# Kernel optimization log

Measured on AMD Instinct MI355X. Metric: run time of the kernel, lower is better.

Reference implementation:

```python
import jax, jax.numpy as jnp
import numpy as np

VOCAB = 200000
D = 128
B, P, R = 256, 64, 32
EPS = 1e-8


def _cos(a, b):
    # torch CosineSimilarity(dim=-1, eps=1e-8): clamp norms
    na = jnp.maximum(jnp.linalg.norm(a, axis=-1), EPS)
    nb = jnp.maximum(jnp.linalg.norm(b, axis=-1), EPS)
    return jnp.sum(a * b, axis=-1) / (na * nb)


def setup_inputs() -> dict:
    key = jax.random.key(0)
    ks = jax.random.split(key, 16)
    s = 1.0 / np.sqrt(D)
    inp = {
        "support_path": jax.random.randint(ks[0], (B, P, 3), 0, VOCAB - 1),
        "support_pair": jax.random.randint(ks[1], (B, 2), 0, VOCAB - 1),
        "support_relation_set": jax.random.randint(ks[2], (B, R), 0, VOCAB - 1),
        "emb": jax.random.normal(ks[3], (VOCAB, D), jnp.float32),
        "w_d_w": jax.random.uniform(ks[4], (D, D), jnp.float32, -s, s),
        "w_d_b": jax.random.uniform(ks[5], (D,), jnp.float32, -s, s),
        "w_e_w": jax.random.uniform(ks[6], (D, D), jnp.float32, -s, s),
        "w_e_b": jax.random.uniform(ks[7], (D,), jnp.float32, -s, s),
        "w_p_w": jax.random.uniform(ks[8], (D, D), jnp.float32, -s, s),
        "w_p_b": jax.random.uniform(ks[9], (D,), jnp.float32, -s, s),
        "e_u_w": jax.random.uniform(ks[10], (1, D), jnp.float32, -s, s),
        "e_u_b": jax.random.uniform(ks[11], (1,), jnp.float32, -s, s),
        "gru_w_ih": jax.random.uniform(ks[12], (3 * D, D), jnp.float32, -s, s),
        "gru_w_hh": jax.random.uniform(ks[13], (3 * D, D), jnp.float32, -s, s),
        "gru_b_ih": jax.random.uniform(ks[14], (3 * D,), jnp.float32, -s, s),
        "gru_b_hh": jax.random.uniform(ks[15], (3 * D,), jnp.float32, -s, s),
    }
    return inp


def _gru_cell(x, h, w_ih, w_hh, b_ih, b_hh):
    gi = x @ w_ih.T + b_ih
    gh = h @ w_hh.T + b_hh
    i_r, i_z, i_n = jnp.split(gi, 3, axis=-1)
    h_r, h_z, h_n = jnp.split(gh, 3, axis=-1)
    r = jax.nn.sigmoid(i_r + h_r)
    z = jax.nn.sigmoid(i_z + h_z)
    n = jnp.tanh(i_n + r * h_n)
    return (1.0 - z) * n + z * h


def reference(support_path, support_pair, support_relation_set, emb,
              w_d_w, w_d_b, w_e_w, w_e_b, w_p_w, w_p_b,
              e_u_w, e_u_b, gru_w_ih, gru_w_hh, gru_b_ih, gru_b_hh):
    head_emb = emb[support_pair[:, 0]]          # [B, D]
    tail_emb = emb[support_pair[:, 1]]          # [B, D]
    hts = _cos(head_emb, tail_emb)              # [B], head-tail sim per group

    rel_emb = emb[support_path]                 # [B, P, 3, D] per-step relation embeddings
    relset_emb = emb[support_relation_set]      # [B, R, D]

    # attention denominator over the group's relation set
    exp_set = jnp.exp(relset_emb @ e_u_w.T + e_u_b)        # [B, R, 1]
    sum_exp = jnp.sum(exp_set, axis=1, keepdims=True)      # [B, 1, 1]

    # entity_1/entity_2 are read from the path tensor in the original code
    e1 = rel_emb[:, :, 0, :]                                # [B, P, D]
    e2 = rel_emb[:, :, 1, :]
    h_b = head_emb[:, None, :]                              # [B, 1, D]
    t_b = tail_emb[:, None, :]
    sim_e1 = 0.5 * (_cos(h_b, e1) + _cos(t_b, e1))          # [B, P]
    sim_e2 = 0.5 * (_cos(h_b, e2) + _cos(t_b, e2))
    hts_b = hts[:, None]
    sim_rel = jnp.stack([
        0.5 * (hts_b + sim_e1),
        0.5 * (sim_e1 + sim_e2),
        0.5 * (hts_b + sim_e2),
    ], axis=-1)                                             # [B, P, 3]
    sim_dist = (1.0 - sim_rel) / 2.0                        # [B, P, 3]

    # attention score per path step
    e_score = jnp.exp(rel_emb @ e_u_w.T + e_u_b) / sum_exp[:, :, None, :]  # [B, P, 3, 1]

    d_in = rel_emb * sim_dist[..., None]
    e_in = rel_emb * e_score
    d_out = d_in @ w_d_w.T + w_d_b
    e_out = e_in @ w_e_w.T + w_e_b
    cost = 0.001 * jax.nn.relu(d_out + e_out)               # [B, P, 3, D]

    # GRU over 3 path steps, zero initial hidden
    rel_in = (rel_emb - cost) @ w_p_w.T + w_p_b             # [B, P, 3, D]
    x_steps = jnp.moveaxis(rel_in.reshape(B * P, 3, D), 1, 0)  # [3, B*P, D]

    def step(h, x):
        h2 = _gru_cell(x, h, gru_w_ih, gru_w_hh, gru_b_ih, gru_b_hh)
        return h2, None

    h0 = jnp.zeros((B * P, D), rel_in.dtype)
    h_final, _ = jax.lax.scan(step, h0, x_steps)
    return h_final.reshape(B, P, D)
```

## Files before the change

### kernel.cpp

```cpp
#include <hip/hip_runtime.h>
#include <cmath>

#define D_ 128
#define B_ 256
#define P_ 64
#define R_ 32
#define GROWS 192
#define EPS_ 1e-8f

typedef unsigned short u16;
typedef unsigned int   u32;
using bf16x8 = __attribute__((ext_vector_type(8))) __bf16;
using f32x4  = __attribute__((ext_vector_type(4))) float;

__device__ __forceinline__ float sigm_f(float x){ return 1.0f/(1.0f + __expf(-x)); }
__device__ __forceinline__ float tanh_f(float x){
    float e = __expf(2.0f*x);
    return 1.0f - 2.0f/(e + 1.0f);
}

__device__ __forceinline__ u16 f2b(float f){
    u32 u = __builtin_bit_cast(u32, f);
    u += 0x7fffu + ((u >> 16) & 1u);
    return (u16)(u >> 16);
}
__device__ __forceinline__ float b2f(u16 s){
    return __builtin_bit_cast(float, ((u32)s) << 16);
}
__device__ __forceinline__ bf16x8 pack8(float a0,float a1,float a2,float a3,
                                        float a4,float a5,float a6,float a7){
    uint4 r;
    r.x = (u32)f2b(a0) | ((u32)f2b(a1) << 16);
    r.y = (u32)f2b(a2) | ((u32)f2b(a3) << 16);
    r.z = (u32)f2b(a4) | ((u32)f2b(a5) << 16);
    r.w = (u32)f2b(a6) | ((u32)f2b(a7) << 16);
    return __builtin_bit_cast(bf16x8, r);
}
__device__ __forceinline__ bf16x8 ldg8(const u16* p){
    return __builtin_bit_cast(bf16x8, *(const uint4*)p);
}
__device__ __forceinline__ bf16x8 ldA(const u16* Xs, int row, int gk){
    return __builtin_bit_cast(bf16x8,
        *(const uint4*)(&Xs[row*128 + ((gk ^ (row & 7)) << 3)]));
}
__device__ __forceinline__ int swz_slot(int row, int col){
    return row*128 + (((col >> 3) ^ (row & 7)) << 3) + (col & 7);
}

__global__ __launch_bounds__(1024) void k_wcvt(
    const float* __restrict__ wd, const float* __restrict__ we,
    const float* __restrict__ wp, const float* __restrict__ wih,
    const float* __restrict__ whh,
    u16* __restrict__ wdb, u16* __restrict__ web, u16* __restrict__ wpb,
    u16* __restrict__ wib, u16* __restrict__ whb)
{
    int i = blockIdx.x*1024 + threadIdx.x;
    int e = i*8;
    const float* src; u16* dst; int off;
    if      (e < 16384) { src = wd;  dst = wdb; off = e; }
    else if (e < 32768) { src = we;  dst = web; off = e - 16384; }
    else if (e < 49152) { src = wp;  dst = wpb; off = e - 32768; }
    else if (e < 98304) { src = wih; dst = wib; off = e - 49152; }
    else                { src = whh; dst = whb; off = e - 98304; }
    float4 a = *(const float4*)(src + off);
    float4 b = *(const float4*)(src + off + 4);
    uint4 r;
    r.x = (u32)f2b(a.x) | ((u32)f2b(a.y) << 16);
    r.y = (u32)f2b(a.z) | ((u32)f2b(a.w) << 16);
    r.z = (u32)f2b(b.x) | ((u32)f2b(b.y) << 16);
    r.w = (u32)f2b(b.z) | ((u32)f2b(b.w) << 16);
    *(uint4*)(dst + off) = r;
}

__global__ __launch_bounds__(512,2) void k_mega(
    const int* __restrict__ pair, const int* __restrict__ relset,
    const int* __restrict__ path,
    const float* __restrict__ emb, const float* __restrict__ eu,
    const float* __restrict__ eub,
    const u16* __restrict__ wdb, const float* __restrict__ bd,
    const u16* __restrict__ web, const float* __restrict__ be,
    const u16* __restrict__ wpb, const float* __restrict__ bpv_,
    const u16* __restrict__ wib, const u16* __restrict__ whb,
    const float* __restrict__ bih, const float* __restrict__ bhh,
    float* __restrict__ out)
{
    __shared__ u16   Xs[GROWS*128];
    __shared__ u16   X2[GROWS*128];
    __shared__ u16   Hs[64*128];
    __shared__ int   pS[GROWS];
    __shared__ float pdh[GROWS], pdt[GROWS], pdu[GROWS], pnn[GROWS];
    __shared__ float sdS[GROWS], seS[GROWS];
    __shared__ float s_hts, s_hi, s_ti;
    __shared__ float s_part[8];

    const int b    = blockIdx.x;
    const int tid  = threadIdx.x;
    const int wave = tid >> 6, lane = tid & 63;
    const int lrow = lane & 15, lk8 = lane >> 4;
    const int col  = wave*16 + lrow;
    const float eb = eub[0];

    if (tid < GROWS) pS[tid] = path[b*GROWS + tid];
    bf16x8 fD[4], fE[4];
    #pragma unroll
    for (int ks = 0; ks < 4; ++ks) {
        const int gk = ks*4 + lk8;
        fD[ks] = ldg8(wdb + col*128 + gk*8);
        fE[ks] = ldg8(web + col*128 + gk*8);
    }
    const int ph = pair[2*b], ptl = pair[2*b+1];
    __syncthreads();

    {
        #pragma unroll
        for (int i = 0; i < 6; ++i) {
            int gid = i*512 + tid;
            int r = gid >> 4, g = gid & 15;
            const float* sp = emb + (size_t)pS[r]*128 + g*8;
            float4 f0 = *(const float4*)sp;
            float4 f1 = *(const float4*)(sp + 4);
            bf16x8 v = pack8(f0.x,f0.y,f0.z,f0.w, f1.x,f1.y,f1.z,f1.w);
            *(uint4*)(&Xs[r*128 + ((g ^ (r & 7)) << 3)]) = __builtin_bit_cast(uint4, v);
        }
        if (wave == 0) {
            float2 hv2 = *(const float2*)(emb + (size_t)ph*128 + 2*lane);
            float2 tv2 = *(const float2*)(emb + (size_t)ptl*128 + 2*lane);
            float dht = hv2.x*tv2.x + hv2.y*tv2.y;
            float dhh = hv2.x*hv2.x + hv2.y*hv2.y;
            float dtt = tv2.x*tv2.x + tv2.y*tv2.y;
            #pragma unroll
            for (int o = 32; o > 0; o >>= 1) {
                dht += __shfl_xor(dht, o);
                dhh += __shfl_xor(dhh, o);
                dtt += __shfl_xor(dtt, o);
            }
            if (lane == 0) {
                float hn = 1.f / fmaxf(sqrtf(dhh), EPS_);
                float tn = 1.f / fmaxf(sqrtf(dtt), EPS_);
                s_hts = dht*hn*tn;
                s_hi  = hn;
                s_ti  = tn;
            }
        }
        float2 uv2 = *(const float2*)(eu + 2*lane);
        float accs = 0.f;
        #pragma unroll
        for (int k = 0; k < 4; ++k) {
            const int ri = relset[b*R_ + wave*4 + k];
            float2 ev = *(const float2*)(emb + (size_t)ri*128 + 2*lane);
            float du = ev.x*uv2.x + ev.y*uv2.y;
            #pragma unroll
            for (int o = 32; o > 0; o >>= 1) du += __shfl_xor(du, o);
            accs += __expf(du + eb);
        }
        if (lane == 0) s_part[wave] = accs;
    }
    __syncthreads();

    {
        const int sub = lane >> 4, l16 = lane & 15;
        const float* hpq = emb + (size_t)ph*128  + l16*8;
        const float* tpq = emb + (size_t)ptl*128 + l16*8;
        const float* upq = eu + l16*8;
        float hq[8], tq[8], uq[8];
        {
            float4 a0 = *(const float4*)hpq, a1 = *(const float4*)(hpq+4);
            float4 b0 = *(const float4*)tpq, b1 = *(const float4*)(tpq+4);
            float4 c0 = *(const float4*)upq, c1 = *(const float4*)(upq+4);
            hq[0]=a0.x;hq[1]=a0.y;hq[2]=a0.z;hq[3]=a0.w;hq[4]=a1.x;hq[5]=a1.y;hq[6]=a1.z;hq[7]=a1.w;
            tq[0]=b0.x;tq[1]=b0.y;tq[2]=b0.z;tq[3]=b0.w;tq[4]=b1.x;tq[5]=b1.y;tq[6]=b1.z;tq[7]=b1.w;
            uq[0]=c0.x;uq[1]=c0.y;uq[2]=c0.z;uq[3]=c0.w;uq[4]=c1.x;uq[5]=c1.y;uq[6]=c1.z;uq[7]=c1.w;
        }
        #pragma unroll
        for (int i = 0; i < 6; ++i) {
            const int r = wave*24 + i*4 + sub;
            uint4 gv = *(const uint4*)(&Xs[r*128 + ((l16 ^ (r & 7)) << 3)]);
            float v[8];
            v[0]=b2f((u16)(gv.x&0xffff)); v[1]=b2f((u16)(gv.x>>16));
            v[2]=b2f((u16)(gv.y&0xffff)); v[3]=b2f((u16)(gv.y>>16));
            v[4]=b2f((u16)(gv.z&0xffff)); v[5]=b2f((u16)(gv.z>>16));
            v[6]=b2f((u16)(gv.w&0xffff)); v[7]=b2f((u16)(gv.w>>16));
            float dh=0.f, dt=0.f, du=0.f, nn=0.f;
            #pragma unroll
            for (int j = 0; j < 8; ++j) {
                dh = fmaf(v[j], hq[j], dh);
                dt = fmaf(v[j], tq[j], dt);
                du = fmaf(v[j], uq[j], du);
                nn = fmaf(v[j], v[j], nn);
            }
            #pragma unroll
            for (int o = 8; o > 0; o >>= 1) {
                dh += __shfl_xor(dh, o);
                dt += __shfl_xor(dt, o);
                du += __shfl_xor(du, o);
                nn += __shfl_xor(nn, o);
            }
            if (l16 == 0) { pdh[r]=dh; pdt[r]=dt; pdu[r]=du; pnn[r]=nn; }
        }
    }
    __syncthreads();

    if (tid < 64) {
        float is = 0.f;
        #pragma unroll
        for (int w = 0; w < 8; ++w) is += s_part[w];
        is = 1.f/is;
        const float hi = s_hi, ti = s_ti, ht = s_hts;
        const int r1 = 3*tid, r2 = r1+1, r3 = r1+2;
        float n1i = 1.f / fmaxf(sqrtf(pnn[r1]), EPS_);
        float n2i = 1.f / fmaxf(sqrtf(pnn[r2]), EPS_);
        float se1 = 0.5f*(pdh[r1]*hi + pdt[r1]*ti)*n1i;
        float se2 = 0.5f*(pdh[r2]*hi + pdt[r2]*ti)*n2i;
        sdS[r1] = (1.f - 0.5f*(ht  + se1))*0.5f;
        sdS[r2] = (1.f - 0.5f*(se1 + se2))*0.5f;
        sdS[r3] = (1.f - 0.5f*(ht  + se2))*0.5f;
        seS[r1] = expf(pdu[r1] + eb)*is;
        seS[r2] = expf(pdu[r2] + eb)*is;
        seS[r3] = expf(pdu[r3] + eb)*is;
    }
    __syncthreads();

    {
        const float bde = bd[col] + be[col];
        #pragma unroll 2
        for (int mt = 0; mt < 12; ++mt) {
            f32x4 aD = (f32x4){0,0,0,0}, aE = (f32x4){0,0,0,0};
            #pragma unroll
            for (int ks = 0; ks < 4; ++ks) {
                const int gk = ks*4 + lk8;
                bf16x8 a = ldA(Xs, mt*16 + lrow, gk);
                aD = __builtin_amdgcn_mfma_f32_16x16x32_bf16(a, fD[ks], aD, 0,0,0);
                aE = __builtin_amdgcn_mfma_f32_16x16x32_bf16(a, fE[ks], aE, 0,0,0);
            }
            #pragma unroll
            for (int rr = 0; rr < 4; ++rr) {
                const int row = mt*16 + lk8*4 + rr;
                const int sl  = swz_slot(row, col);
                float relv = b2f(Xs[sl]);
                float c = sdS[row]*aD[rr] + seS[row]*aE[rr] + bde;
                X2[sl] = f2b(relv - 1e-3f*fmaxf(c, 0.f));
            }
        }
    }
    __syncthreads();

    {
        bf16x8 fP[4];
        #pragma unroll
        for (int ks = 0; ks < 4; ++ks)
            fP[ks] = ldg8(wpb + col*128 + (ks*4 + lk8)*8);
        const float bpv = bpv_[col];
        #pragma unroll 2
        for (int mt = 0; mt < 12; ++mt) {
            f32x4 aP = (f32x4){0,0,0,0};
            #pragma unroll
            for (int ks = 0; ks < 4; ++ks) {
                const int gk = ks*4 + lk8;
                bf16x8 a = ldA(X2, mt*16 + lrow, gk);
                aP = __builtin_amdgcn_mfma_f32_16x16x32_bf16(a, fP[ks], aP, 0,0,0);
            }
            #pragma unroll
            for (int rr = 0; rr < 4; ++rr) {
                const int row = mt*16 + lk8*4 + rr;
                Xs[swz_slot(row, col)] = f2b(aP[rr] + bpv);
            }
        }
    }

    bf16x8 wR[4], wZ[4], wI[4];
    #pragma unroll
    for (int ks = 0; ks < 4; ++ks) {
        const int gk = ks*4 + lk8;
        wR[ks] = ldg8(wib +           col*128 + gk*8);
        wZ[ks] = ldg8(wib + 16384   + col*128 + gk*8);
        wI[ks] = ldg8(wib + 2*16384 + col*128 + gk*8);
    }
    const float brv = bih[col]       + bhh[col];
    const float bzv = bih[128 + col] + bhh[128 + col];
    const float biN = bih[256 + col];
    const float bhN = bhh[256 + col];
    __syncthreads();

    float hreg[4][4];
    f32x4 aR[4], aZ[4], aI[4], aH[4];

    #pragma unroll
    for (int m = 0; m < 4; ++m) { aR[m]=(f32x4){0,0,0,0}; aZ[m]=(f32x4){0,0,0,0}; aI[m]=(f32x4){0,0,0,0}; }
    #pragma unroll
    for (int ks = 0; ks < 4; ++ks) {
        const int gk = ks*4 + lk8;
        #pragma unroll
        for (int mt = 0; mt < 4; ++mt) {
            bf16x8 ax = ldA(Xs, 3*(mt*16 + lrow) + 0, gk);
            aR[mt] = __builtin_amdgcn_mfma_f32_16x16x32_bf16(ax, wR[ks], aR[mt], 0,0,0);
            aZ[mt] = __builtin_amdgcn_mfma_f32_16x16x32_bf16(ax, wZ[ks], aZ[mt], 0,0,0);
            aI[mt] = __builtin_amdgcn_mfma_f32_16x16x32_bf16(ax, wI[ks], aI[mt], 0,0,0);
        }
    }
    #pragma unroll
    for (int mt = 0; mt < 4; ++mt)
        #pragma unroll
        for (int rr = 0; rr < 4; ++rr) {
            const int row = mt*16 + lk8*4 + rr;
            float rv = sigm_f(aR[mt][rr] + brv);
            float zv = sigm_f(aZ[mt][rr] + bzv);
            float nn = tanh_f(aI[mt][rr] + biN + rv*bhN);
            float h2 = (1.f - zv)*nn;
            hreg[mt][rr] = h2;
            Hs[swz_slot(row, col)] = f2b(h2);
        }
    __syncthreads();

    #pragma unroll
    for (int t = 1; t < 3; ++t) {
        #pragma unroll
        for (int m = 0; m < 4; ++m) { aR[m]=(f32x4){0,0,0,0}; aZ[m]=(f32x4){0,0,0,0}; aI[m]=(f32x4){0,0,0,0}; aH[m]=(f32x4){0,0,0,0}; }
        #pragma unroll
        for (int ks = 0; ks < 4; ++ks) {
            const int gk = ks*4 + lk8;
            bf16x8 vRk = ldg8(whb +           col*128 + gk*8);
            bf16x8 vZk = ldg8(whb + 16384   + col*128 + gk*8);
            bf16x8 vHk = ldg8(whb + 2*16384 + col*128 + gk*8);
            #pragma unroll
            for (int mt = 0; mt < 4; ++mt) {
                bf16x8 ax = ldA(Xs, 3*(mt*16 + lrow) + t, gk);
                bf16x8 ah = ldA(Hs, mt*16 + lrow, gk);
                aR[mt] = __builtin_amdgcn_mfma_f32_16x16x32_bf16(ax, wR[ks], aR[mt], 0,0,0);
                aZ[mt] = __builtin_amdgcn_mfma_f32_16x16x32_bf16(ax, wZ[ks], aZ[mt], 0,0,0);
                aI[mt] = __builtin_amdgcn_mfma_f32_16x16x32_bf16(ax, wI[ks], aI[mt], 0,0,0);
                aR[mt] = __builtin_amdgcn_mfma_f32_16x16x32_bf16(ah, vRk, aR[mt], 0,0,0);
                aZ[mt] = __builtin_amdgcn_mfma_f32_16x16x32_bf16(ah, vZk, aZ[mt], 0,0,0);
                aH[mt] = __builtin_amdgcn_mfma_f32_16x16x32_bf16(ah, vHk, aH[mt], 0,0,0);
            }
        }
        __syncthreads();
        if (t < 2) {
            #pragma unroll
            for (int mt = 0; mt < 4; ++mt)
                #pragma unroll
                for (int rr = 0; rr < 4; ++rr) {
                    const int row = mt*16 + lk8*4 + rr;
                    float rv = sigm_f(aR[mt][rr] + brv);
                    float zv = sigm_f(aZ[mt][rr] + bzv);
                    float hn = aH[mt][rr] + bhN;
                    float nn = tanh_f(aI[mt][rr] + biN + rv*hn);
                    float h2 = (1.f - zv)*nn + zv*hreg[mt][rr];
                    hreg[mt][rr] = h2;
                    Hs[swz_slot(row, col)] = f2b(h2);
                }
            __syncthreads();
        } else {
            const int bp0 = b*64;
            #pragma unroll
            for (int mt = 0; mt < 4; ++mt)
                #pragma unroll
                for (int rr = 0; rr < 4; ++rr) {
                    const int row = mt*16 + lk8*4 + rr;
                    float rv = sigm_f(aR[mt][rr] + brv);
                    float zv = sigm_f(aZ[mt][rr] + bzv);
                    float hn = aH[mt][rr] + bhN;
                    float nn = tanh_f(aI[mt][rr] + biN + rv*hn);
                    float h2 = (1.f - zv)*nn + zv*hreg[mt][rr];
                    out[(size_t)(bp0 + row)*128 + col] = h2;
                }
        }
    }
}

extern "C" void kernel_launch(void* const* d_in, const int* in_sizes, int n_in,
                              void* d_out, int out_size, void* d_ws, size_t ws_size,
                              hipStream_t stream)
{
    const int*   path   = (const int*)d_in[0];
    const int*   pair   = (const int*)d_in[1];
    const int*   relset = (const int*)d_in[2];
    const float* emb    = (const float*)d_in[3];
    const float* wd     = (const float*)d_in[4];
    const float* bd     = (const float*)d_in[5];
    const float* we     = (const float*)d_in[6];
    const float* be     = (const float*)d_in[7];
    const float* wp     = (const float*)d_in[8];
    const float* bp     = (const float*)d_in[9];
    const float* eu     = (const float*)d_in[10];
    const float* eub    = (const float*)d_in[11];
    const float* wih    = (const float*)d_in[12];
    const float* whh    = (const float*)d_in[13];
    const float* bih    = (const float*)d_in[14];
    const float* bhh    = (const float*)d_in[15];
    float* out = (float*)d_out;
    float* ws  = (float*)d_ws;

    u16* wdb = (u16*)ws;
    u16* web = wdb + 16384;
    u16* wpb = web + 16384;
    u16* wib = wpb + 16384;
    u16* whb = wib + 49152;

    k_wcvt<<<18, 1024, 0, stream>>>(wd, we, wp, wih, whh, wdb, web, wpb, wib, whb);
    k_mega<<<B_, 512, 0, stream>>>(pair, relset, path, emb, eu, eub,
                                   wdb, bd, web, be, wpb, bp,
                                   wib, whb, bih, bhh, out);
}
```

Measured before the change: 44.23 us.

## Split each batch item across two blocks, halving path rows per block

Measured after the change: 56.65 us. 1.28x slower.

```diff
diff --git a/kernel.cpp b/kernel.cpp
--- a/kernel.cpp
+++ b/kernel.cpp
@@ -5,7 +5,7 @@
 #define B_ 256
 #define P_ 64
 #define R_ 32
-#define GROWS 192
+#define HROWS 96
 #define EPS_ 1e-8f
 
 typedef unsigned short u16;
@@ -84,23 +84,25 @@
     const float* __restrict__ bih, const float* __restrict__ bhh,
     float* __restrict__ out)
 {
-    __shared__ u16   Xs[GROWS*128];
-    __shared__ u16   X2[GROWS*128];
-    __shared__ u16   Hs[64*128];
-    __shared__ int   pS[GROWS];
-    __shared__ float pdh[GROWS], pdt[GROWS], pdu[GROWS], pnn[GROWS];
-    __shared__ float sdS[GROWS], seS[GROWS];
+    __shared__ u16   Xs[HROWS*128];
+    __shared__ u16   X2[HROWS*128];
+    __shared__ u16   Hs[32*128];
+    __shared__ int   pS[HROWS];
+    __shared__ float pdh[HROWS], pdt[HROWS], pdu[HROWS], pnn[HROWS];
+    __shared__ float sdS[HROWS], seS[HROWS];
     __shared__ float s_hts, s_hi, s_ti;
     __shared__ float s_part[8];
 
-    const int b    = blockIdx.x;
+    const int blk  = blockIdx.x;
+    const int b    = blk >> 1;
+    const int hb   = blk & 1;
     const int tid  = threadIdx.x;
     const int wave = tid >> 6, lane = tid & 63;
     const int lrow = lane & 15, lk8 = lane >> 4;
     const int col  = wave*16 + lrow;
     const float eb = eub[0];
 
-    if (tid < GROWS) pS[tid] = path[b*GROWS + tid];
+    if (tid < HROWS) pS[tid] = path[b*192 + hb*HROWS + tid];
     bf16x8 fD[4], fE[4];
     #pragma unroll
     for (int ks = 0; ks < 4; ++ks) {
@@ -113,7 +115,7 @@
 
     {
         #pragma unroll
-        for (int i = 0; i < 6; ++i) {
+        for (int i = 0; i < 3; ++i) {
             int gid = i*512 + tid;
             int r = gid >> 4, g = gid & 15;
             const float* sp = emb + (size_t)pS[r]*128 + g*8;
@@ -158,7 +160,8 @@
     __syncthreads();
 
     {
-        const int sub = lane >> 4, l16 = lane & 15;
+        const int grp = tid >> 4;
+        const int l16 = tid & 15;
         const float* hpq = emb + (size_t)ph*128  + l16*8;
         const float* tpq = emb + (size_t)ptl*128 + l16*8;
         const float* upq = eu + l16*8;
@@ -172,8 +175,8 @@
             uq[0]=c0.x;uq[1]=c0.y;uq[2]=c0.z;uq[3]=c0.w;uq[4]=c1.x;uq[5]=c1.y;uq[6]=c1.z;uq[7]=c1.w;
         }
         #pragma unroll
-        for (int i = 0; i < 6; ++i) {
-            const int r = wave*24 + i*4 + sub;
+        for (int i = 0; i < 3; ++i) {
+            const int r = i*32 + grp;
             uint4 gv = *(const uint4*)(&Xs[r*128 + ((l16 ^ (r & 7)) << 3)]);
             float v[8];
             v[0]=b2f((u16)(gv.x&0xffff)); v[1]=b2f((u16)(gv.x>>16));
@@ -200,7 +203,7 @@
     }
     __syncthreads();
 
-    if (tid < 64) {
+    if (tid < 32) {
         float is = 0.f;
         #pragma unroll
         for (int w = 0; w < 8; ++w) is += s_part[w];
@@ -214,16 +217,16 @@
         sdS[r1] = (1.f - 0.5f*(ht  + se1))*0.5f;
         sdS[r2] = (1.f - 0.5f*(se1 + se2))*0.5f;
         sdS[r3] = (1.f - 0.5f*(ht  + se2))*0.5f;
-        seS[r1] = expf(pdu[r1] + eb)*is;
-        seS[r2] = expf(pdu[r2] + eb)*is;
-        seS[r3] = expf(pdu[r3] + eb)*is;
+        seS[r1] = __expf(pdu[r1] + eb)*is;
+        seS[r2] = __expf(pdu[r2] + eb)*is;
+        seS[r3] = __expf(pdu[r3] + eb)*is;
     }
     __syncthreads();
 
     {
         const float bde = bd[col] + be[col];
         #pragma unroll 2
-        for (int mt = 0; mt < 12; ++mt) {
+        for (int mt = 0; mt < 6; ++mt) {
             f32x4 aD = (f32x4){0,0,0,0}, aE = (f32x4){0,0,0,0};
             #pragma unroll
             for (int ks = 0; ks < 4; ++ks) {
@@ -251,7 +254,7 @@
             fP[ks] = ldg8(wpb + col*128 + (ks*4 + lk8)*8);
         const float bpv = bpv_[col];
         #pragma unroll 2
-        for (int mt = 0; mt < 12; ++mt) {
+        for (int mt = 0; mt < 6; ++mt) {
             f32x4 aP = (f32x4){0,0,0,0};
             #pragma unroll
             for (int ks = 0; ks < 4; ++ks) {
@@ -281,16 +284,16 @@
     const float bhN = bhh[256 + col];
     __syncthreads();
 
-    float hreg[4][4];
-    f32x4 aR[4], aZ[4], aI[4], aH[4];
-
-    #pragma unroll
-    for (int m = 0; m < 4; ++m) { aR[m]=(f32x4){0,0,0,0}; aZ[m]=(f32x4){0,0,0,0}; aI[m]=(f32x4){0,0,0,0}; }
+    float hreg[2][4];
+    f32x4 aR[2], aZ[2], aI[2], aH[2];
+
+    #pragma unroll
+    for (int m = 0; m < 2; ++m) { aR[m]=(f32x4){0,0,0,0}; aZ[m]=(f32x4){0,0,0,0}; aI[m]=(f32x4){0,0,0,0}; }
     #pragma unroll
     for (int ks = 0; ks < 4; ++ks) {
         const int gk = ks*4 + lk8;
         #pragma unroll
-        for (int mt = 0; mt < 4; ++mt) {
+        for (int mt = 0; mt < 2; ++mt) {
             bf16x8 ax = ldA(Xs, 3*(mt*16 + lrow) + 0, gk);
             aR[mt] = __builtin_amdgcn_mfma_f32_16x16x32_bf16(ax, wR[ks], aR[mt], 0,0,0);
             aZ[mt] = __builtin_amdgcn_mfma_f32_16x16x32_bf16(ax, wZ[ks], aZ[mt], 0,0,0);
@@ -298,7 +301,7 @@
         }
     }
     #pragma unroll
-    for (int mt = 0; mt < 4; ++mt)
+    for (int mt = 0; mt < 2; ++mt)
         #pragma unroll
         for (int rr = 0; rr < 4; ++rr) {
             const int row = mt*16 + lk8*4 + rr;
@@ -314,7 +317,7 @@
     #pragma unroll
     for (int t = 1; t < 3; ++t) {
         #pragma unroll
-        for (int m = 0; m < 4; ++m) { aR[m]=(f32x4){0,0,0,0}; aZ[m]=(f32x4){0,0,0,0}; aI[m]=(f32x4){0,0,0,0}; aH[m]=(f32x4){0,0,0,0}; }
+        for (int m = 0; m < 2; ++m) { aR[m]=(f32x4){0,0,0,0}; aZ[m]=(f32x4){0,0,0,0}; aI[m]=(f32x4){0,0,0,0}; aH[m]=(f32x4){0,0,0,0}; }
         #pragma unroll
         for (int ks = 0; ks < 4; ++ks) {
             const int gk = ks*4 + lk8;
@@ -322,7 +325,7 @@
             bf16x8 vZk = ldg8(whb + 16384   + col*128 + gk*8);
             bf16x8 vHk = ldg8(whb + 2*16384 + col*128 + gk*8);
             #pragma unroll
-            for (int mt = 0; mt < 4; ++mt) {
+            for (int mt = 0; mt < 2; ++mt) {
                 bf16x8 ax = ldA(Xs, 3*(mt*16 + lrow) + t, gk);
                 bf16x8 ah = ldA(Hs, mt*16 + lrow, gk);
                 aR[mt] = __builtin_amdgcn_mfma_f32_16x16x32_bf16(ax, wR[ks], aR[mt], 0,0,0);
@@ -336,7 +339,7 @@
         __syncthreads();
         if (t < 2) {
             #pragma unroll
-            for (int mt = 0; mt < 4; ++mt)
+            for (int mt = 0; mt < 2; ++mt)
                 #pragma unroll
                 for (int rr = 0; rr < 4; ++rr) {
                     const int row = mt*16 + lk8*4 + rr;
@@ -350,9 +353,9 @@
                 }
             __syncthreads();
         } else {
-            const int bp0 = b*64;
-            #pragma unroll
-            for (int mt = 0; mt < 4; ++mt)
+            const int bp0 = b*64 + hb*32;
+            #pragma unroll
+            for (int mt = 0; mt < 2; ++mt)
                 #pragma unroll
                 for (int rr = 0; rr < 4; ++rr) {
                     const int row = mt*16 + lk8*4 + rr;
@@ -397,7 +400,7 @@
     u16* whb = wib + 49152;
 
     k_wcvt<<<18, 1024, 0, stream>>>(wd, we, wp, wih, whh, wdb, web, wpb, wib, whb);
-    k_mega<<<B_, 512, 0, stream>>>(pair, relset, path, emb, eu, eub,
-                                   wdb, bd, web, be, wpb, bp,
-                                   wib, whb, bih, bhh, out);
-}
+    k_mega<<<2*B_, 512, 0, stream>>>(pair, relset, path, emb, eu, eub,
+                                     wdb, bd, web, be, wpb, bp,
+                                     wib, whb, bih, bhh, out);
+}
```
